# Kernel tuning notes

Measured on AMD Instinct MI355X. Metric: run time of the kernel, lower is better.

## Reference

```python
import jax, jax.numpy as jnp
import numpy as np

V_MIN = -10.0
V_MAX = 10.0
NUM_ATOMS = 51
ATOM_DELTA = (V_MAX - V_MIN) / (NUM_ATOMS - 1)
BS = 1_000_000


def setup_inputs() -> dict:
    key = jax.random.key(0)
    k1, k2 = jax.random.split(key)
    reward = jax.random.normal(k1, (BS,), dtype=jnp.float32) * 3.0
    probs = jax.random.uniform(k2, (BS, NUM_ATOMS), dtype=jnp.float32)
    atom_values = (V_MIN + ATOM_DELTA * jnp.arange(NUM_ATOMS)).astype(jnp.float32)
    return {"reward": reward, "probs": probs, "atom_values": atom_values}


def reference(reward, probs, atom_values):
    # Categorical (C51) Bellman projection, expressed as a scatter-add
    # instead of the original's dense [bs, A, A] projection matrix + bmm.
    bs, A = probs.shape
    # shifted & clamped atom support: [bs, A]
    new_vals = jnp.clip(atom_values[None, :] + reward[:, None], V_MIN, V_MAX)
    idx = (new_vals - V_MIN) / ATOM_DELTA           # fractional atom index
    lower = jnp.floor(idx)
    upper = jnp.ceil(idx)
    same = lower == upper                           # idx landed exactly on an atom
    l_coef = jnp.where(same, 1.0, upper - idx)      # original sets 1.0 when l == u
    u_coef = idx - lower                            # 0 when same
    li = lower.astype(jnp.int32)
    ui = upper.astype(jnp.int32)
    rows = jnp.broadcast_to(jnp.arange(bs)[:, None], (bs, A))
    out = jnp.zeros_like(probs)
    out = out.at[rows, li].add(l_coef * probs)
    out = out.at[rows, ui].add(u_coef * probs)
    return out
```

## Files before the change

### kernel.cpp

```cpp
#include <hip/hip_runtime.h>

#define NA 51
#define ROWS 256
#define STRIDE 53

__global__ __launch_bounds__(256, 1) void c51_bellman_kernel(
    const float* __restrict__ reward,
    const float* __restrict__ probs,
    float* __restrict__ out,
    int bs)
{
    __shared__ float lds[ROWS * STRIDE];
    const int tid  = threadIdx.x;
    const int row0 = blockIdx.x * ROWS;
    const int nrows = min(ROWS, bs - row0);
    const int nelem = nrows * NA;
    const int n4    = nelem >> 2;

    if (tid < nrows) {
        lds[tid * STRIDE]          = 0.0f;
        lds[tid * STRIDE + NA + 1] = 0.0f;
    }

    const float4* p4 = (const float4*)(probs + (size_t)row0 * NA);
    for (int e4 = tid; e4 < n4; e4 += ROWS) {
        float4 v = p4[e4];
        unsigned g = (unsigned)e4 * 4u;
        unsigned r0 = g / 51u, j0 = g - r0 * 51u;
        float vv[4] = {v.x, v.y, v.z, v.w};
        #pragma unroll
        for (int c = 0; c < 4; ++c) {
            unsigned r = r0, j = j0 + c;
            if (j >= 51u) { j -= 51u; r += 1u; }
            lds[r * STRIDE + 1 + j] = vv[c];
        }
    }
    for (int e = (n4 << 2) + tid; e < nelem; e += ROWS) {
        unsigned r = (unsigned)e / 51u, j = (unsigned)e - r * 51u;
        lds[r * STRIDE + 1 + j] = probs[(size_t)row0 * NA + e];
    }
    __syncthreads();

    const bool active = (tid < nrows);
    float* rp = &lds[tid * STRIDE + 1];
    if (active) {
        const float s  = reward[row0 + tid] * 2.5f;
        const float kf = floorf(s);
        const int   k  = (int)kf;
        const float f  = s - kf;

        float m_lo = 0.0f, m_hi = 0.0f;
        #pragma unroll
        for (int j = 0; j < NA; ++j) {
            const float pj = rp[j];
            const float t  = (float)j + s;
            if (t < 0.0f)  m_lo += pj;
            if (t > 50.0f) m_hi += pj;
        }

        const bool down = (k >= 0);
        #pragma unroll
        for (int m = 0; m < NA; ++m) {
            const int i  = down ? (NA - 1 - m) : m;
            const int j2 = i - k - 1;
            const int j1 = j2 + 1;
            const int c  = min(max(j2, -1), NA - 1);
            const float plo = rp[c];
            const float phi = rp[c + 1];
            float o = 0.0f;
            if (j1 >= 0 && j1 < NA && ((float)i + f) <= 50.0f)
                o += (1.0f - f) * phi;
            if (j2 >= 0 && j2 < NA && ((float)(i - 1) + f) >= 0.0f)
                o += f * plo;
            if (i == 0)      o += m_lo;
            if (i == NA - 1) o += m_hi;
            rp[i] = o;
        }
    }
    __syncthreads();

    float4* o4 = (float4*)(out + (size_t)row0 * NA);
    for (int e4 = tid; e4 < n4; e4 += ROWS) {
        unsigned g = (unsigned)e4 * 4u;
        unsigned r0 = g / 51u, j0 = g - r0 * 51u;
        float vv[4];
        #pragma unroll
        for (int c = 0; c < 4; ++c) {
            unsigned r = r0, j = j0 + c;
            if (j >= 51u) { j -= 51u; r += 1u; }
            vv[c] = lds[r * STRIDE + 1 + j];
        }
        float4 v; v.x = vv[0]; v.y = vv[1]; v.z = vv[2]; v.w = vv[3];
        o4[e4] = v;
    }
    for (int e = (n4 << 2) + tid; e < nelem; e += ROWS) {
        unsigned r = (unsigned)e / 51u, j = (unsigned)e - r * 51u;
        out[(size_t)row0 * NA + e] = lds[r * STRIDE + 1 + j];
    }
}

extern "C" void kernel_launch(void* const* d_in, const int* in_sizes, int n_in,
                              void* d_out, int out_size, void* d_ws, size_t ws_size,
                              hipStream_t stream) {
    const float* reward = (const float*)d_in[0];
    const float* probs  = (const float*)d_in[1];
    float* out = (float*)d_out;
    const int bs = in_sizes[0];

    const int blocks = (bs + ROWS - 1) / ROWS;
    c51_bellman_kernel<<<blocks, ROWS, 0, stream>>>(reward, probs, out, bs);
}
```

Before: 422.2 us.

## Use unpadded LDS layout with float4 copies and register-buffered projection

Drops the padded stride-53 shared-memory layout in favour of a contiguous stride-51 layout. The global-to-LDS and LDS-to-global copies become plain float4 moves with no per-element divide and remap. The projection loop now keeps a rolling previous value and writes its results to a register array before storing them back, so it no longer has to be ordered to avoid in-place overwrite. Launch bounds are raised to 3 blocks per CU to allow more occupancy. The trade-offs are possible LDS bank conflicts from the odd stride in the per-row phase and higher register pressure from the 51-entry array.

```diff
diff --git a/kernel.cpp b/kernel.cpp
--- a/kernel.cpp
+++ b/kernel.cpp
@@ -2,52 +2,33 @@
 
 #define NA 51
 #define ROWS 256
-#define STRIDE 53
 
-__global__ __launch_bounds__(256, 1) void c51_bellman_kernel(
+__global__ __launch_bounds__(256, 3) void c51_bellman_kernel(
     const float* __restrict__ reward,
     const float* __restrict__ probs,
     float* __restrict__ out,
     int bs)
 {
-    __shared__ float lds[ROWS * STRIDE];
-    const int tid  = threadIdx.x;
-    const int row0 = blockIdx.x * ROWS;
+    __shared__ float lds[ROWS * NA];
+    const int tid   = threadIdx.x;
+    const int row0  = blockIdx.x * ROWS;
     const int nrows = min(ROWS, bs - row0);
     const int nelem = nrows * NA;
     const int n4    = nelem >> 2;
 
-    if (tid < nrows) {
-        lds[tid * STRIDE]          = 0.0f;
-        lds[tid * STRIDE + NA + 1] = 0.0f;
-    }
-
     const float4* p4 = (const float4*)(probs + (size_t)row0 * NA);
-    for (int e4 = tid; e4 < n4; e4 += ROWS) {
-        float4 v = p4[e4];
-        unsigned g = (unsigned)e4 * 4u;
-        unsigned r0 = g / 51u, j0 = g - r0 * 51u;
-        float vv[4] = {v.x, v.y, v.z, v.w};
-        #pragma unroll
-        for (int c = 0; c < 4; ++c) {
-            unsigned r = r0, j = j0 + c;
-            if (j >= 51u) { j -= 51u; r += 1u; }
-            lds[r * STRIDE + 1 + j] = vv[c];
-        }
-    }
-    for (int e = (n4 << 2) + tid; e < nelem; e += ROWS) {
-        unsigned r = (unsigned)e / 51u, j = (unsigned)e - r * 51u;
-        lds[r * STRIDE + 1 + j] = probs[(size_t)row0 * NA + e];
-    }
+    float4* l4 = (float4*)lds;
+    for (int e4 = tid; e4 < n4; e4 += ROWS) l4[e4] = p4[e4];
+    for (int e = (n4 << 2) + tid; e < nelem; e += ROWS)
+        lds[e] = probs[(size_t)row0 * NA + e];
     __syncthreads();
 
-    const bool active = (tid < nrows);
-    float* rp = &lds[tid * STRIDE + 1];
-    if (active) {
+    if (tid < nrows) {
         const float s  = reward[row0 + tid] * 2.5f;
         const float kf = floorf(s);
         const int   k  = (int)kf;
         const float f  = s - kf;
+        const float* rp = lds + tid * NA;
 
         float m_lo = 0.0f, m_hi = 0.0f;
         #pragma unroll
@@ -58,45 +39,39 @@
             if (t > 50.0f) m_hi += pj;
         }
 
-        const bool down = (k >= 0);
+        float o[NA];
+        float prev;
+        {
+            const int jm = -k - 1;
+            const int cm = min(max(jm, 0), NA - 1);
+            const float v = rp[cm];
+            prev = (jm >= 0 && jm < NA) ? v : 0.0f;
+        }
         #pragma unroll
-        for (int m = 0; m < NA; ++m) {
-            const int i  = down ? (NA - 1 - m) : m;
-            const int j2 = i - k - 1;
-            const int j1 = j2 + 1;
-            const int c  = min(max(j2, -1), NA - 1);
-            const float plo = rp[c];
-            const float phi = rp[c + 1];
-            float o = 0.0f;
-            if (j1 >= 0 && j1 < NA && ((float)i + f) <= 50.0f)
-                o += (1.0f - f) * phi;
-            if (j2 >= 0 && j2 < NA && ((float)(i - 1) + f) >= 0.0f)
-                o += f * plo;
-            if (i == 0)      o += m_lo;
-            if (i == NA - 1) o += m_hi;
-            rp[i] = o;
+        for (int i = 0; i < NA; ++i) {
+            const int j = i - k;
+            const int c = min(max(j, 0), NA - 1);
+            const float v = rp[c];
+            const float cur = (j >= 0 && j < NA) ? v : 0.0f;
+            const float w1 = ((float)i + f <= 50.0f) ? (1.0f - f) : 0.0f;
+            const float w2 = ((float)(i - 1) + f >= 0.0f) ? f : 0.0f;
+            o[i] = w1 * cur + w2 * prev;
+            prev = cur;
         }
+        o[0]      += m_lo;
+        o[NA - 1] += m_hi;
+
+        float* wp = lds + tid * NA;
+        #pragma unroll
+        for (int i = 0; i < NA; ++i) wp[i] = o[i];
     }
     __syncthreads();
 
     float4* o4 = (float4*)(out + (size_t)row0 * NA);
-    for (int e4 = tid; e4 < n4; e4 += ROWS) {
-        unsigned g = (unsigned)e4 * 4u;
-        unsigned r0 = g / 51u, j0 = g - r0 * 51u;
-        float vv[4];
-        #pragma unroll
-        for (int c = 0; c < 4; ++c) {
-            unsigned r = r0, j = j0 + c;
-            if (j >= 51u) { j -= 51u; r += 1u; }
-            vv[c] = lds[r * STRIDE + 1 + j];
-        }
-        float4 v; v.x = vv[0]; v.y = vv[1]; v.z = vv[2]; v.w = vv[3];
-        o4[e4] = v;
-    }
-    for (int e = (n4 << 2) + tid; e < nelem; e += ROWS) {
-        unsigned r = (unsigned)e / 51u, j = (unsigned)e - r * 51u;
-        out[(size_t)row0 * NA + e] = lds[r * STRIDE + 1 + j];
-    }
+    const float4* l4c = (const float4*)lds;
+    for (int e4 = tid; e4 < n4; e4 += ROWS) o4[e4] = l4c[e4];
+    for (int e = (n4 << 2) + tid; e < nelem; e += ROWS)
+        out[(size_t)row0 * NA + e] = lds[e];
 }
 
 extern "C" void kernel_launch(void* const* d_in, const int* in_sizes, int n_in,
```

After: 365.5 us. 13.4% less time.
